# Optimization experiments

Measured on AMD Instinct MI355X. Metric: run time of the kernel, lower is better.

The kernel has to match this reference:

```python
import jax, jax.numpy as jnp
import numpy as np

C = 1.0
SQRT_C = 1.0
EPS = 1e-6

N_NODES = 50000
N_EDGES = 800000
IN_F = 128   # in_features (weight columns); x has IN_F+1 coords
OUT_F = 128  # out_features; output has OUT_F coords


def l_inner(x, y):
    # Lorentz inner product: -x0*y0 + sum_i xi*yi
    return jnp.sum(x[..., 1:] * y[..., 1:], axis=-1) - x[..., 0] * y[..., 0]


def arcosh(z):
    z = jnp.maximum(z, 1.0 + 1e-7)
    return jnp.log(z + jnp.sqrt(z * z - 1.0))


def log_map_zero(y):
    # log map at origin o=(sqrt(c),0,...,0); result is tangent with head 0
    dist = SQRT_C * arcosh(y[..., 0] / SQRT_C)                      # [N]
    tail = y[..., 1:]
    tail_norm = jnp.sqrt(jnp.maximum(jnp.sum(tail * tail, -1), EPS))
    scaled = (dist / tail_norm)[..., None] * tail
    return jnp.concatenate([jnp.zeros_like(y[..., :1]), scaled], -1)


def exp_map_zero(v):
    # v is a tangent vector at the origin with head component 0
    tail = v[..., 1:]
    n = jnp.sqrt(jnp.maximum(jnp.sum(tail * tail, -1, keepdims=True), EPS))
    n_cut = jnp.minimum(n, 50.0)
    new_tail = SQRT_C * jnp.sinh(n_cut / SQRT_C) * tail / n
    # project onto the hyperboloid: x0 = sqrt(c + ||tail||^2)
    head = jnp.sqrt(C + jnp.sum(new_tail * new_tail, -1, keepdims=True))
    return jnp.concatenate([head, new_tail], -1)


def matvec_regular(weight, x, bias):
    # LGCNLinear forward (eval mode: dropout is identity)
    x_tan = log_map_zero(x)                      # [N, IN_F+1], head = 0
    mx = x_tan[..., 1:] @ weight.T + bias        # [N, OUT_F-1]
    v = jnp.concatenate([x_tan[..., :1], mx], -1)  # head stays 0 (tangent-zero normalized)
    return exp_map_zero(v)                       # [N, OUT_F]


def lorentz_centroid(x, row, col, val):
    # sparse spmm aggregation + Lorentz centroid renormalization
    n = x.shape[0]
    msgs = val[:, None] * x[col]                               # [E, OUT_F] gather
    s = jax.ops.segment_sum(msgs, row, num_segments=n)         # [N, OUT_F] scatter-add
    inner = l_inner(s, s)                                      # [N]
    coef = SQRT_C / jnp.sqrt(jnp.maximum(jnp.abs(inner), EPS))
    return coef[:, None] * s


def hyp_act(x):
    # HypAct: log-map, relu in tangent space, exp-map (c_in == c_out)
    xt = jax.nn.relu(log_map_zero(x))  # head 0 -> relu keeps it 0
    return exp_map_zero(xt)


def setup_inputs() -> dict:
    key = jax.random.key(0)
    k1, k2, k3, k4, k5, k6 = jax.random.split(key, 6)
    tail = 0.5 * jax.random.normal(k1, (N_NODES, IN_F), dtype=jnp.float32)
    head = jnp.sqrt(C + jnp.sum(tail * tail, -1, keepdims=True))
    x = jnp.concatenate([head, tail], -1)                       # on-hyperboloid points
    weight = jax.random.normal(k2, (OUT_F - 1, IN_F), dtype=jnp.float32) * (1.0 / np.sqrt(IN_F))
    bias = 0.01 * jax.random.normal(k3, (OUT_F - 1,), dtype=jnp.float32)
    adj_val = jax.random.uniform(k4, (N_EDGES,), dtype=jnp.float32) / 16.0
    adj_row = jnp.sort(jax.random.randint(k5, (N_EDGES,), 0, N_NODES, dtype=jnp.int32))
    adj_col = jax.random.randint(k6, (N_EDGES,), 0, N_NODES, dtype=jnp.int32)
    return {"x": x, "weight": weight, "bias": bias, "adj_val": adj_val,
            "adj_row": adj_row, "adj_col": adj_col}


def reference(x, weight, bias, adj_val, adj_row, adj_col):
    h = matvec_regular(weight, x, bias)          # hyperbolic linear
    h = lorentz_centroid(h, adj_row, adj_col, adj_val)  # sparse agg + centroid
    h = hyp_act(h)                               # hyperbolic activation
    return h
```

## Files before the change

### kernel.cpp

```cpp
#include <hip/hip_runtime.h>
#include <hip/hip_bf16.h>

#define NN 50000
#define NE 800000

typedef __attribute__((ext_vector_type(4))) float f32x4;
typedef __attribute__((ext_vector_type(8))) __bf16 bf16x8;

__device__ __forceinline__ float wred64(float v) {
    v += __shfl_xor(v, 32, 64);
    v += __shfl_xor(v, 16, 64);
    v += __shfl_xor(v, 8, 64);
    v += __shfl_xor(v, 4, 64);
    v += __shfl_xor(v, 2, 64);
    v += __shfl_xor(v, 1, 64);
    return v;
}

__device__ __forceinline__ float arcosh_f(float z) {
    z = fmaxf(z, 1.0f + 1e-7f);
    return logf(z + sqrtf(z * z - 1.0f));
}

__global__ void prep_kernel(const float* __restrict__ weight, const float* __restrict__ bias,
                            ushort* __restrict__ WfHi, ushort* __restrict__ WfLo,
                            float* __restrict__ biasP) {
    int t8 = blockIdx.x * 256 + threadIdx.x;
    int l = t8 & 63, f = t8 >> 6;
    int t = f & 3, jt = f >> 2;
    int g = l >> 4, r = l & 15;
    int col = jt * 16 + r;
    #pragma unroll
    for (int i = 0; i < 8; ++i) {
        int k = 32 * g + 8 * t + i;
        float v = (col < 127) ? weight[col * 128 + k] : 0.0f;
        __bf16 h = (__bf16)v;
        float lo = v - (float)h;
        __bf16 lb = (__bf16)lo;
        WfHi[t8 * 8 + i] = __builtin_bit_cast(unsigned short, h);
        WfLo[t8 * 8 + i] = __builtin_bit_cast(unsigned short, lb);
    }
    if (t8 < 128) biasP[t8] = (t8 < 127) ? bias[t8] : 0.0f;
}

__global__ void rowptr_kernel(const int* __restrict__ row, int* __restrict__ rowptr) {
    int e = blockIdx.x * 256 + threadIdx.x;
    if (e >= NE) return;
    int r1 = row[e];
    int r0 = (e == 0) ? -1 : row[e - 1];
    for (int r = r0 + 1; r <= r1; ++r) rowptr[r] = e;
    if (e == NE - 1) {
        for (int r = r1 + 1; r <= NN; ++r) rowptr[r] = NE;
    }
}

__global__ __launch_bounds__(256) void transform_kernel(
        const float* __restrict__ x, const ushort* __restrict__ Wf ,
        const float* __restrict__ biasP, ushort* __restrict__ hhb,
        float* __restrict__ hhead) {
    __shared__ __align__(16) ushort WF[32768];

    const int tid = threadIdx.x;
    #pragma unroll
    for (int i = 0; i < 16; ++i)
        ((float4*)WF)[i * 256 + tid] = ((const float4*)Wf)[i * 256 + tid];

    const int lane = tid & 63, w = tid >> 6;
    const int g = lane >> 4, r = lane & 15;
    const int nodeA = blockIdx.x * 64 + w * 16 + r;

    float xv[32];
    float x0 = 1.0f;
    if (nodeA < NN) {
        const float* xp = x + (long)nodeA * 129;
        x0 = xp[0];
        __builtin_memcpy(xv, xp + 1 + 32 * g, 128);
    } else {
        #pragma unroll
        for (int i = 0; i < 32; ++i) xv[i] = 0.0f;
    }
    float dist = arcosh_f(x0);
    float sc = dist / sqrtf(fmaxf(x0 * x0 - 1.0f, 1e-6f));

    bf16x8 ah[4], al[4];
    #pragma unroll
    for (int t = 0; t < 4; ++t) {
        #pragma unroll
        for (int i = 0; i < 8; ++i) {
            float v = sc * xv[8 * t + i];
            __bf16 h = (__bf16)v;
            ah[t][i] = h;
            al[t][i] = (__bf16)(v - (float)h);
        }
    }
    __syncthreads();

    f32x4 acc[8];
    #pragma unroll
    for (int jt = 0; jt < 8; ++jt) acc[jt] = (f32x4){0.0f, 0.0f, 0.0f, 0.0f};

    #pragma unroll
    for (int jt = 0; jt < 8; ++jt) {
        #pragma unroll
        for (int t = 0; t < 4; ++t) {
            const int f = jt * 4 + t;
            bf16x8 bh = *(const bf16x8*)&WF[(f * 64 + lane) * 8];
            bf16x8 bl = *(const bf16x8*)&WF[16384 + (f * 64 + lane) * 8];
            acc[jt] = __builtin_amdgcn_mfma_f32_16x16x32_bf16(al[t], bh, acc[jt], 0, 0, 0);
            acc[jt] = __builtin_amdgcn_mfma_f32_16x16x32_bf16(ah[t], bl, acc[jt], 0, 0, 0);
            acc[jt] = __builtin_amdgcn_mfma_f32_16x16x32_bf16(ah[t], bh, acc[jt], 0, 0, 0);
        }
    }

    float bv[8];
    #pragma unroll
    for (int jt = 0; jt < 8; ++jt) bv[jt] = biasP[jt * 16 + r];

    #pragma unroll
    for (int i = 0; i < 4; ++i) {
        float m[8];
        float p = 0.0f;
        #pragma unroll
        for (int jt = 0; jt < 8; ++jt) {
            m[jt] = acc[jt][i] + bv[jt];
            p = fmaf(m[jt], m[jt], p);
        }
        p += __shfl_xor(p, 1, 64);
        p += __shfl_xor(p, 2, 64);
        p += __shfl_xor(p, 4, 64);
        p += __shfl_xor(p, 8, 64);
        float n = sqrtf(fmaxf(p, 1e-6f));
        float rr = sinhf(fminf(n, 50.0f)) / n;
        int node = blockIdx.x * 64 + w * 16 + g * 4 + i;
        if (node < NN) {
            #pragma unroll
            for (int jt = 0; jt < 8; ++jt) {
                int j = jt * 16 + r;
                float vv = rr * m[jt];
                ushort us = (j == 127) ? (ushort)0
                          : __builtin_bit_cast(unsigned short, (__bf16)vv);
                hhb[node * 128 + j] = us;
            }
            if (r == 15) hhead[node] = sqrtf(1.0f + rr * rr * p);
        }
    }
}

__global__ __launch_bounds__(256) void centroid_act_kernel(
        const ushort* __restrict__ hhb, const float* __restrict__ hhead,
        const float* __restrict__ val, const int* __restrict__ col,
        const int* __restrict__ rowptr, float* __restrict__ out) {
    const int lane = threadIdx.x & 63;
    const int node = __builtin_amdgcn_readfirstlane(blockIdx.x * 4 + (threadIdx.x >> 6));
    const int lo = __builtin_amdgcn_readfirstlane(rowptr[node]);
    const int hi = __builtin_amdgcn_readfirstlane(rowptr[node + 1]);

    float s0 = 0.0f, sf0 = 0.0f, sf1 = 0.0f;
    int e = lo;
    for (; e + 8 <= hi; e += 8) {
        int c[8]; float v[8];
        #pragma unroll
        for (int k = 0; k < 8; ++k) { c[k] = col[e + k]; v[k] = val[e + k]; }
        uint u[8]; float hd[8];
        #pragma unroll
        for (int k = 0; k < 8; ++k) {
            u[k]  = *(const uint*)&hhb[((long)c[k] << 7) + 2 * lane];
            hd[k] = hhead[c[k]];
        }
        #pragma unroll
        for (int k = 0; k < 8; ++k) {
            float f0 = __builtin_bit_cast(float, u[k] << 16);
            float f1 = __builtin_bit_cast(float, u[k] & 0xffff0000u);
            sf0 = fmaf(v[k], f0, sf0);
            sf1 = fmaf(v[k], f1, sf1);
            s0  = fmaf(v[k], hd[k], s0);
        }
    }
    for (; e < hi; ++e) {
        int c = col[e]; float v = val[e];
        uint u = *(const uint*)&hhb[((long)c << 7) + 2 * lane];
        sf0 = fmaf(v, __builtin_bit_cast(float, u << 16), sf0);
        sf1 = fmaf(v, __builtin_bit_cast(float, u & 0xffff0000u), sf1);
        s0  = fmaf(v, hhead[c], s0);
    }

    float tsum = wred64(sf0 * sf0 + sf1 * sf1);
    float inner = tsum - s0 * s0;
    float coef = 1.0f / sqrtf(fmaxf(fabsf(inner), 1e-6f));
    float h20 = coef * s0;

    float dist = arcosh_f(h20);
    float tsq = coef * coef * tsum;
    float scl = dist / sqrtf(fmaxf(tsq, 1e-6f));
    float u0 = fmaxf(scl * coef * sf0, 0.0f);
    float u1 = fmaxf(scl * coef * sf1, 0.0f);
    float S = wred64(u0 * u0 + u1 * u1);
    float n = sqrtf(fmaxf(S, 1e-6f));
    float r = sinhf(fminf(n, 50.0f)) / n;

    float* op = out + (long)node * 128;
    op[1 + 2 * lane] = r * u0;
    if (lane < 63) op[2 + 2 * lane] = r * u1;
    else           op[0] = sqrtf(1.0f + r * r * S);
}

extern "C" void kernel_launch(void* const* d_in, const int* in_sizes, int n_in,
                              void* d_out, int out_size, void* d_ws, size_t ws_size,
                              hipStream_t stream) {
    const float* x       = (const float*)d_in[0];
    const float* weight  = (const float*)d_in[1];
    const float* bias    = (const float*)d_in[2];
    const float* adj_val = (const float*)d_in[3];
    const int*   adj_row = (const int*)d_in[4];
    const int*   adj_col = (const int*)d_in[5];
    float* out = (float*)d_out;

    char* ws = (char*)d_ws;
    ushort* hhb    = (ushort*)ws;
    float*  hhead  = (float*)(ws + 12800000);
    int*    rowptr = (int*)(ws + 13000000);
    ushort* WfHi   = (ushort*)(ws + 13200192);
    ushort* WfLo   = (ushort*)(ws + 13232960);
    float*  biasP  = (float*)(ws + 13265728);

    prep_kernel<<<8, 256, 0, stream>>>(weight, bias, WfHi, WfLo, biasP);
    rowptr_kernel<<<(NE + 255) / 256, 256, 0, stream>>>(adj_row, rowptr);
    transform_kernel<<<(NN + 63) / 64, 256, 0, stream>>>(x, WfHi, biasP, hhb, hhead);
    centroid_act_kernel<<<NN / 4, 256, 0, stream>>>(hhb, hhead, adj_val, adj_col, rowptr, out);
}
```

Measured before the change: 78.56 us.

## Process four edges per wavefront with 16-byte row loads in centroid gather

The centroid kernel now splits each wavefront into four 16-lane groups, each handling a different edge and loading its full bf16 feature row with one 16-byte load per lane instead of one 4-byte load per lane per edge. Partial sums are combined across groups with cross-lane shuffles and the head sum is divided by 16 to undo the redundant per-lane accumulation. This is meant to issue wider, fewer memory requests and cut per-edge loop overhead. In exchange it drops the 8-edge unrolling, so fewer loads are in flight per iteration, and it adds shuffle reductions and a more complex output mapping.

After: 77.80 us. No clear change (-1.0%).

```diff
diff --git a/kernel.cpp b/kernel.cpp
--- a/kernel.cpp
+++ b/kernel.cpp
@@ -151,57 +151,80 @@
         const float* __restrict__ val, const int* __restrict__ col,
         const int* __restrict__ rowptr, float* __restrict__ out) {
     const int lane = threadIdx.x & 63;
-    const int node = __builtin_amdgcn_readfirstlane(blockIdx.x * 4 + (threadIdx.x >> 6));
-    const int lo = __builtin_amdgcn_readfirstlane(rowptr[node]);
-    const int hi = __builtin_amdgcn_readfirstlane(rowptr[node + 1]);
-
-    float s0 = 0.0f, sf0 = 0.0f, sf1 = 0.0f;
-    int e = lo;
-    for (; e + 8 <= hi; e += 8) {
-        int c[8]; float v[8];
-        #pragma unroll
-        for (int k = 0; k < 8; ++k) { c[k] = col[e + k]; v[k] = val[e + k]; }
-        uint u[8]; float hd[8];
-        #pragma unroll
-        for (int k = 0; k < 8; ++k) {
-            u[k]  = *(const uint*)&hhb[((long)c[k] << 7) + 2 * lane];
-            hd[k] = hhead[c[k]];
-        }
-        #pragma unroll
-        for (int k = 0; k < 8; ++k) {
-            float f0 = __builtin_bit_cast(float, u[k] << 16);
-            float f1 = __builtin_bit_cast(float, u[k] & 0xffff0000u);
-            sf0 = fmaf(v[k], f0, sf0);
-            sf1 = fmaf(v[k], f1, sf1);
-            s0  = fmaf(v[k], hd[k], s0);
-        }
-    }
-    for (; e < hi; ++e) {
-        int c = col[e]; float v = val[e];
-        uint u = *(const uint*)&hhb[((long)c << 7) + 2 * lane];
-        sf0 = fmaf(v, __builtin_bit_cast(float, u << 16), sf0);
-        sf1 = fmaf(v, __builtin_bit_cast(float, u & 0xffff0000u), sf1);
-        s0  = fmaf(v, hhead[c], s0);
-    }
-
-    float tsum = wred64(sf0 * sf0 + sf1 * sf1);
-    float inner = tsum - s0 * s0;
-    float coef = 1.0f / sqrtf(fmaxf(fabsf(inner), 1e-6f));
-    float h20 = coef * s0;
-
-    float dist = arcosh_f(h20);
-    float tsq = coef * coef * tsum;
-    float scl = dist / sqrtf(fmaxf(tsq, 1e-6f));
-    float u0 = fmaxf(scl * coef * sf0, 0.0f);
-    float u1 = fmaxf(scl * coef * sf1, 0.0f);
-    float S = wred64(u0 * u0 + u1 * u1);
-    float n = sqrtf(fmaxf(S, 1e-6f));
-    float r = sinhf(fminf(n, 50.0f)) / n;
-
+    const int node = blockIdx.x * 4 + (threadIdx.x >> 6);
+    const int g = lane >> 4, r = lane & 15;
+    const int lo = rowptr[node], hi = rowptr[node + 1];
+
+    float sf[8];
+    #pragma unroll
+    for (int j = 0; j < 8; ++j) sf[j] = 0.0f;
+    float s0p = 0.0f;
+
+    for (int e = lo; e < hi; e += 4) {
+        const int m = hi - e;
+        const int idx = e + ((g < m) ? g : (m - 1));
+        const int cg = col[idx];
+        const float vg = (g < m) ? val[idx] : 0.0f;
+
+        s0p = fmaf(vg, hhead[cg], s0p);
+
+        const uint4 u = *(const uint4*)&hhb[((long)cg << 7) + r * 8];
+        sf[0] = fmaf(vg, __builtin_bit_cast(float, u.x << 16), sf[0]);
+        sf[1] = fmaf(vg, __builtin_bit_cast(float, u.x & 0xffff0000u), sf[1]);
+        sf[2] = fmaf(vg, __builtin_bit_cast(float, u.y << 16), sf[2]);
+        sf[3] = fmaf(vg, __builtin_bit_cast(float, u.y & 0xffff0000u), sf[3]);
+        sf[4] = fmaf(vg, __builtin_bit_cast(float, u.z << 16), sf[4]);
+        sf[5] = fmaf(vg, __builtin_bit_cast(float, u.z & 0xffff0000u), sf[5]);
+        sf[6] = fmaf(vg, __builtin_bit_cast(float, u.w << 16), sf[6]);
+        sf[7] = fmaf(vg, __builtin_bit_cast(float, u.w & 0xffff0000u), sf[7]);
+    }
+
+    #pragma unroll
+    for (int j = 0; j < 8; ++j) {
+        sf[j] += __shfl_xor(sf[j], 16, 64);
+        sf[j] += __shfl_xor(sf[j], 32, 64);
+    }
+    float s0 = wred64(s0p) * 0.0625f;
+
+    float p2 = 0.0f;
+    #pragma unroll
+    for (int j = 0; j < 8; ++j) p2 = fmaf(sf[j], sf[j], p2);
+    p2 += __shfl_xor(p2, 1, 64);
+    p2 += __shfl_xor(p2, 2, 64);
+    p2 += __shfl_xor(p2, 4, 64);
+    p2 += __shfl_xor(p2, 8, 64);
+    const float tsum = p2;
+
+    const float inner = tsum - s0 * s0;
+    const float coef = 1.0f / sqrtf(fmaxf(fabsf(inner), 1e-6f));
+    const float h20 = coef * s0;
+
+    const float dist = arcosh_f(h20);
+    const float tsq = coef * coef * tsum;
+    const float scl = dist / sqrtf(fmaxf(tsq, 1e-6f));
+
+    float uu[8];
+    float p3 = 0.0f;
+    #pragma unroll
+    for (int j = 0; j < 8; ++j) {
+        uu[j] = fmaxf(scl * coef * sf[j], 0.0f);
+        p3 = fmaf(uu[j], uu[j], p3);
+    }
+    p3 += __shfl_xor(p3, 1, 64);
+    p3 += __shfl_xor(p3, 2, 64);
+    p3 += __shfl_xor(p3, 4, 64);
+    p3 += __shfl_xor(p3, 8, 64);
+    const float S = p3;
+    const float n = sqrtf(fmaxf(S, 1e-6f));
+    const float rr = sinhf(fminf(n, 50.0f)) / n;
+
+    const float ua = (g < 2) ? ((g == 0) ? uu[0] : uu[2]) : ((g == 2) ? uu[4] : uu[6]);
+    const float ub = (g < 2) ? ((g == 0) ? uu[1] : uu[3]) : ((g == 2) ? uu[5] : uu[7]);
+    const int c1 = r * 8 + 2 * g;
     float* op = out + (long)node * 128;
-    op[1 + 2 * lane] = r * u0;
-    if (lane < 63) op[2 + 2 * lane] = r * u1;
-    else           op[0] = sqrtf(1.0f + r * r * S);
+    op[1 + c1] = rr * ua;
+    if (c1 + 1 < 127) op[2 + c1] = rr * ub;
+    else              op[0] = sqrtf(1.0f + rr * rr * S);
 }
 
 extern "C" void kernel_launch(void* const* d_in, const int* in_sizes, int n_in,
```

## Fuse prep and rowptr kernels; restructure centroid edge loop with lane-parallel head sum

Applied to the files above, without the earlier changes.

Merges the weight-prep and rowptr construction into one launch split by block index, which removes one kernel launch. In the centroid kernel, the head-coordinate sum is now computed lane-parallel over edges and then reduced across the wave, instead of every lane redundantly loading hhead per edge. The edge loop drops its scalar remainder loop and instead pads the last batch of 8 with clamped indices and zero weights, using 32-bit offsets. This trades a few redundant loads on the tail batch for fewer instructions and less duplicated memory traffic.

After: 69.81 us. -11.1%, faster.

```diff
diff --git a/kernel.cpp b/kernel.cpp
--- a/kernel.cpp
+++ b/kernel.cpp
@@ -22,35 +22,38 @@
     return logf(z + sqrtf(z * z - 1.0f));
 }
 
-__global__ void prep_kernel(const float* __restrict__ weight, const float* __restrict__ bias,
-                            ushort* __restrict__ WfHi, ushort* __restrict__ WfLo,
-                            float* __restrict__ biasP) {
-    int t8 = blockIdx.x * 256 + threadIdx.x;
-    int l = t8 & 63, f = t8 >> 6;
-    int t = f & 3, jt = f >> 2;
-    int g = l >> 4, r = l & 15;
-    int col = jt * 16 + r;
-    #pragma unroll
-    for (int i = 0; i < 8; ++i) {
-        int k = 32 * g + 8 * t + i;
-        float v = (col < 127) ? weight[col * 128 + k] : 0.0f;
-        __bf16 h = (__bf16)v;
-        float lo = v - (float)h;
-        __bf16 lb = (__bf16)lo;
-        WfHi[t8 * 8 + i] = __builtin_bit_cast(unsigned short, h);
-        WfLo[t8 * 8 + i] = __builtin_bit_cast(unsigned short, lb);
-    }
-    if (t8 < 128) biasP[t8] = (t8 < 127) ? bias[t8] : 0.0f;
-}
-
-__global__ void rowptr_kernel(const int* __restrict__ row, int* __restrict__ rowptr) {
-    int e = blockIdx.x * 256 + threadIdx.x;
-    if (e >= NE) return;
-    int r1 = row[e];
-    int r0 = (e == 0) ? -1 : row[e - 1];
-    for (int r = r0 + 1; r <= r1; ++r) rowptr[r] = e;
-    if (e == NE - 1) {
-        for (int r = r1 + 1; r <= NN; ++r) rowptr[r] = NE;
+__global__ void prep_rowptr_kernel(const float* __restrict__ weight,
+                                   const float* __restrict__ bias,
+                                   ushort* __restrict__ WfHi, ushort* __restrict__ WfLo,
+                                   float* __restrict__ biasP,
+                                   const int* __restrict__ row, int* __restrict__ rowptr) {
+    const int b = blockIdx.x;
+    if (b < 3125) {
+        int e = b * 256 + threadIdx.x;
+        if (e >= NE) return;
+        int r1 = row[e];
+        int r0 = (e == 0) ? -1 : row[e - 1];
+        for (int r = r0 + 1; r <= r1; ++r) rowptr[r] = e;
+        if (e == NE - 1) {
+            for (int r = r1 + 1; r <= NN; ++r) rowptr[r] = NE;
+        }
+    } else {
+        int t8 = (b - 3125) * 256 + threadIdx.x;
+        int l = t8 & 63, f = t8 >> 6;
+        int t = f & 3, jt = f >> 2;
+        int g = l >> 4, r = l & 15;
+        int col = jt * 16 + r;
+        #pragma unroll
+        for (int i = 0; i < 8; ++i) {
+            int k = 32 * g + 8 * t + i;
+            float v = (col < 127) ? weight[col * 128 + k] : 0.0f;
+            __bf16 h = (__bf16)v;
+            float lo = v - (float)h;
+            __bf16 lb = (__bf16)lo;
+            WfHi[t8 * 8 + i] = __builtin_bit_cast(unsigned short, h);
+            WfLo[t8 * 8 + i] = __builtin_bit_cast(unsigned short, lb);
+        }
+        if (t8 < 128) biasP[t8] = (t8 < 127) ? bias[t8] : 0.0f;
     }
 }
 
@@ -152,36 +155,34 @@
         const int* __restrict__ rowptr, float* __restrict__ out) {
     const int lane = threadIdx.x & 63;
     const int node = __builtin_amdgcn_readfirstlane(blockIdx.x * 4 + (threadIdx.x >> 6));
-    const int lo = __builtin_amdgcn_readfirstlane(rowptr[node]);
-    const int hi = __builtin_amdgcn_readfirstlane(rowptr[node + 1]);
-
-    float s0 = 0.0f, sf0 = 0.0f, sf1 = 0.0f;
-    int e = lo;
-    for (; e + 8 <= hi; e += 8) {
+    const int lo = rowptr[node], hi = rowptr[node + 1];
+
+    float s0p = 0.0f;
+    for (int eh = lo + lane; eh < hi; eh += 64) {
+        s0p = fmaf(val[eh], hhead[col[eh]], s0p);
+    }
+    float s0 = wred64(s0p);
+
+    const uint voff = 2u * (uint)lane;
+    float sf0 = 0.0f, sf1 = 0.0f;
+    for (int e = lo; e < hi; e += 8) {
+        const int m = hi - e;
         int c[8]; float v[8];
         #pragma unroll
-        for (int k = 0; k < 8; ++k) { c[k] = col[e + k]; v[k] = val[e + k]; }
-        uint u[8]; float hd[8];
-        #pragma unroll
         for (int k = 0; k < 8; ++k) {
-            u[k]  = *(const uint*)&hhb[((long)c[k] << 7) + 2 * lane];
-            hd[k] = hhead[c[k]];
-        }
+            const int ik = (k < m) ? k : (m - 1);
+            c[k] = col[e + ik];
+            v[k] = (k < m) ? val[e + ik] : 0.0f;
+        }
+        uint u[8];
+        #pragma unroll
+        for (int k = 0; k < 8; ++k)
+            u[k] = *(const uint*)&hhb[(((uint)c[k]) << 7) + voff];
         #pragma unroll
         for (int k = 0; k < 8; ++k) {
-            float f0 = __builtin_bit_cast(float, u[k] << 16);
-            float f1 = __builtin_bit_cast(float, u[k] & 0xffff0000u);
-            sf0 = fmaf(v[k], f0, sf0);
-            sf1 = fmaf(v[k], f1, sf1);
-            s0  = fmaf(v[k], hd[k], s0);
-        }
-    }
-    for (; e < hi; ++e) {
-        int c = col[e]; float v = val[e];
-        uint u = *(const uint*)&hhb[((long)c << 7) + 2 * lane];
-        sf0 = fmaf(v, __builtin_bit_cast(float, u << 16), sf0);
-        sf1 = fmaf(v, __builtin_bit_cast(float, u & 0xffff0000u), sf1);
-        s0  = fmaf(v, hhead[c], s0);
+            sf0 = fmaf(v[k], __builtin_bit_cast(float, u[k] << 16), sf0);
+            sf1 = fmaf(v[k], __builtin_bit_cast(float, u[k] & 0xffff0000u), sf1);
+        }
     }
 
     float tsum = wred64(sf0 * sf0 + sf1 * sf1);
@@ -223,8 +224,8 @@
     ushort* WfLo   = (ushort*)(ws + 13232960);
     float*  biasP  = (float*)(ws + 13265728);
 
-    prep_kernel<<<8, 256, 0, stream>>>(weight, bias, WfHi, WfLo, biasP);
-    rowptr_kernel<<<(NE + 255) / 256, 256, 0, stream>>>(adj_row, rowptr);
+    prep_rowptr_kernel<<<3133, 256, 0, stream>>>(weight, bias, WfHi, WfLo, biasP,
+                                                 adj_row, rowptr);
     transform_kernel<<<(NN + 63) / 64, 256, 0, stream>>>(x, WfHi, biasP, hhb, hhead);
     centroid_act_kernel<<<NN / 4, 256, 0, stream>>>(hhb, hhead, adj_val, adj_col, rowptr, out);
 }
```
